# Performance work log

Measured on AMD Instinct MI355X. Metric: run time of the kernel, lower is better.

Reference implementation:

```python
import jax, jax.numpy as jnp
import numpy as np

B, T, D, H, L, FF, SPLIT = 2, 4096, 256, 4 * 0 + 8, 4, 1024, 2048
HD = D // H
EPS = 1e-5


def _layernorm(x, s, b):
    mu = jnp.mean(x, axis=-1, keepdims=True)
    var = jnp.mean(jnp.square(x - mu), axis=-1, keepdims=True)
    return (x - mu) * jax.lax.rsqrt(var + EPS) * s + b


def setup_inputs() -> dict:
    key = jax.random.key(0)
    ks = jax.random.split(key, 10)
    sc = 0.02
    inp = {
        "rows": jax.random.normal(ks[0], (B, T, D), jnp.float32),
        "train_target_embeddings": jax.random.normal(ks[1], (B, SPLIT, D), jnp.float32),
        "Wq": sc * jax.random.normal(ks[2], (L, D, D), jnp.float32),
        "bq": jnp.zeros((L, D), jnp.float32),
        "Wk": sc * jax.random.normal(ks[3], (L, D, D), jnp.float32),
        "bk": jnp.zeros((L, D), jnp.float32),
        "Wv": sc * jax.random.normal(ks[4], (L, D, D), jnp.float32),
        "bv": jnp.zeros((L, D), jnp.float32),
        "Wo": sc * jax.random.normal(ks[5], (L, D, D), jnp.float32),
        "bo": jnp.zeros((L, D), jnp.float32),
        "W1": sc * jax.random.normal(ks[6], (L, D, FF), jnp.float32),
        "b1": jnp.zeros((L, FF), jnp.float32),
        "W2": sc * jax.random.normal(ks[7], (L, FF, D), jnp.float32),
        "b2": jnp.zeros((L, D), jnp.float32),
        "ln1_s": jnp.ones((L, D), jnp.float32),
        "ln1_b": jnp.zeros((L, D), jnp.float32),
        "ln2_s": jnp.ones((L, D), jnp.float32),
        "ln2_b": jnp.zeros((L, D), jnp.float32),
        "split": SPLIT,
    }
    return inp


def reference(rows, train_target_embeddings, Wq, bq, Wk, bk, Wv, bv, Wo, bo,
              W1, b1, W2, b2, ln1_s, ln1_b, ln2_s, ln2_b, split):
    # residual add of train target embeddings onto the train rows
    x = rows.at[:, :split, :].add(train_target_embeddings)
    t = x.shape[1]
    # allowed mask: every query can see all train columns; test queries also see themselves
    key_is_train = jnp.arange(t) < split                      # [T]
    allowed = key_is_train[None, :] | jnp.eye(t, dtype=bool)  # [T,T]
    neg = jnp.asarray(-1e9, x.dtype)
    scale = 1.0 / np.sqrt(HD)
    n_layers = Wq.shape[0]
    for l in range(n_layers):
        # multi-head attention with structured mask
        q = (x @ Wq[l] + bq[l]).reshape(x.shape[0], t, H, HD)
        k = (x @ Wk[l] + bk[l]).reshape(x.shape[0], t, H, HD)
        v = (x @ Wv[l] + bv[l]).reshape(x.shape[0], t, H, HD)
        logits = jnp.einsum('bqhd,bkhd->bhqk', q, k) * scale
        logits = jnp.where(allowed[None, None], logits, neg)
        attn = jax.nn.softmax(logits, axis=-1)
        o = jnp.einsum('bhqk,bkhd->bqhd', attn, v).reshape(x.shape[0], t, D)
        x = _layernorm(x + (o @ Wo[l] + bo[l]), ln1_s[l], ln1_b[l])
        # feed-forward
        h = jax.nn.gelu(x @ W1[l] + b1[l])
        x = _layernorm(x + (h @ W2[l] + b2[l]), ln2_s[l], ln2_b[l])
    return x
```

## Files before the change

### kernel.cpp

```cpp
#include <hip/hip_runtime.h>
#include <cstdint>
#include <cstddef>

#define TSEQ 4096
#define BATCH 2
#define DIM 256
#define NHEAD 8
#define HDIM 32
#define NLAYER 4
#define FFDIM 1024
#define SPLITN 2048
#define MROWS (BATCH * TSEQ)

#define QSCALE 0.2550784545f

typedef __attribute__((ext_vector_type(4))) float f32x4;
typedef __attribute__((ext_vector_type(8))) short bf16x8;

__device__ __forceinline__ short f2bf(float f) {
  union { float f; uint32_t u; } v; v.f = f;
  uint32_t r = v.u + 0x7fffu + ((v.u >> 16) & 1u);
  return (short)(r >> 16);
}

__device__ __forceinline__ float bf2f(short s) {
  union { uint32_t u; float f; } v; v.u = ((uint32_t)(uint16_t)s) << 16;
  return v.f;
}

__device__ __forceinline__ float fast_exp2(float x) {
#if __has_builtin(__builtin_amdgcn_exp2f)
  return __builtin_amdgcn_exp2f(x);
#else
  float r;
  asm volatile("v_exp_f32 %0, %1\n\ts_nop 1" : "=v"(r) : "v"(x));
  return r;
#endif
}

__device__ __forceinline__ uint32_t pack2bf(float a, float b) {
  union { float f; uint32_t u; } ua, ub; ua.f = a; ub.f = b;
  return ((ua.u + 0x8000u) >> 16) | ((ub.u + 0x8000u) & 0xffff0000u);
}

__device__ __forceinline__ float gelu_f(float x) {
  float u = 0.7978845608f * x * (1.0f + 0.044715f * x * x);
  u = fminf(fmaxf(u, -20.f), 20.f);
  float e = fast_exp2(2.885390082f * u);
  float t = (e - 1.0f) / (e + 1.0f);
  return 0.5f * x * (1.0f + t);
}

#define AS1 __attribute__((address_space(1)))
#define AS3 __attribute__((address_space(3)))
__device__ __forceinline__ void gload16(const void* g, void* l) {
  __builtin_amdgcn_global_load_lds((AS1 void*)g, (AS3 void*)l, 16, 0, 0);
}

__global__ __launch_bounds__(256) void prep_w(
    const float* __restrict__ Wq, const float* __restrict__ Wk,
    const float* __restrict__ Wv, const float* __restrict__ Wo,
    const float* __restrict__ W1, const float* __restrict__ W2,
    short* __restrict__ qkvT, short* __restrict__ woT,
    short* __restrict__ w1T, short* __restrict__ w2T)
{
  const int NQKV = NLAYER * 768 * DIM;
  const int NO   = NLAYER * DIM * DIM;
  const int NF   = NLAYER * FFDIM * DIM;
  const int total = NQKV + NO + 2 * NF;
  for (int idx = blockIdx.x * 256 + threadIdx.x; idx < total; idx += gridDim.x * 256) {
    if (idx < NQKV) {
      const int l = idx / (768 * DIM);
      const int rem = idx - l * 768 * DIM;
      const int n = rem >> 8, k = rem & 255;
      const float* src = (n < 256) ? Wq : ((n < 512) ? Wk : Wv);
      qkvT[idx] = f2bf(src[((size_t)l * DIM + k) * DIM + (n & 255)]);
    } else if (idx < NQKV + NO) {
      const int j = idx - NQKV;
      const int l = j >> 16;
      const int rem = j & 65535;
      const int n = rem >> 8, k = rem & 255;
      woT[j] = f2bf(Wo[((size_t)l * DIM + k) * DIM + n]);
    } else if (idx < NQKV + NO + NF) {
      const int j = idx - NQKV - NO;
      const int l = j >> 18;
      const int rem = j & 262143;
      const int n = rem >> 8, k = rem & 255;
      w1T[j] = f2bf(W1[((size_t)l * DIM + k) * FFDIM + n]);
    } else {
      const int j = idx - NQKV - NO - NF;
      const int l = j >> 18;
      const int rem = j & 262143;
      const int n = rem >> 10, k = rem & 1023;
      w2T[j] = f2bf(W2[((size_t)l * FFDIM + k) * DIM + n]);
    }
  }
}

__global__ __launch_bounds__(256) void prep_x(
    const float* __restrict__ rows, const float* __restrict__ tte,
    float* __restrict__ xf, short* __restrict__ xb)
{
  const size_t idx = (size_t)blockIdx.x * 256 + threadIdx.x;
  float4 v = ((const float4*)rows)[idx];
  const size_t e = idx * 4;
  const int m = (int)(e >> 8);
  const int d = (int)(e & 255);
  const int t = m & (TSEQ - 1);
  const int bb = m >> 12;
  if (t < SPLITN) {
    const float4 a = ((const float4*)tte)[((size_t)bb * SPLITN + t) * (DIM / 4) + (d >> 2)];
    v.x += a.x; v.y += a.y; v.z += a.z; v.w += a.w;
  }
  ((float4*)xf)[idx] = v;
  short4 pk; pk.x = f2bf(v.x); pk.y = f2bf(v.y); pk.z = f2bf(v.z); pk.w = f2bf(v.w);
  ((short4*)xb)[idx] = pk;
}

#define GBM 128
#define GBN 64
#define GBK 64

template<int EPI>
__global__ __launch_bounds__(256, 4) void gemm_bt(
    const short* __restrict__ A, const short* __restrict__ BT,
    const float* __restrict__ bias0, const float* __restrict__ bias1,
    const float* __restrict__ bias2, void* __restrict__ Cout,
    int M, int N, int K)
{
  __shared__ short As[GBM * GBK];
  __shared__ short Bs[GBN * GBK];
  const int tid = threadIdx.x;
  const int lane = tid & 63;
  const int wave = tid >> 6;
  const int wm = wave & 1, wn = wave >> 1;
  const int col = lane & 15, quad = lane >> 4;

  const short* Ab = A + (size_t)blockIdx.x * GBM * K;
  const short* Bb = BT + (size_t)blockIdx.y * GBN * K;

  const f32x4 fz = {0.f, 0.f, 0.f, 0.f};
  f32x4 acc[4][2];
#pragma unroll
  for (int i = 0; i < 4; ++i)
#pragma unroll
    for (int j = 0; j < 2; ++j) acc[i][j] = fz;

  for (int k0 = 0; k0 < K; k0 += GBK) {
#pragma unroll
    for (int p = 0; p < 4; ++p) {
      const int i = p * 256 + tid;
      const int r = i >> 3, g = i & 7;
      gload16(Ab + (size_t)r * K + k0 + ((g ^ (r & 7)) * 8), &As[i * 8]);
    }
#pragma unroll
    for (int p = 0; p < 2; ++p) {
      const int i = p * 256 + tid;
      const int r = i >> 3, g = i & 7;
      gload16(Bb + (size_t)r * K + k0 + ((g ^ (r & 7)) * 8), &Bs[i * 8]);
    }
    __syncthreads();
#pragma unroll
    for (int ks = 0; ks < GBK; ks += 32) {
      bf16x8 af[4], bfr[2];
      const int gq = (ks >> 3) + quad;
#pragma unroll
      for (int tm = 0; tm < 4; ++tm) {
        const int row = wm * 64 + tm * 16 + col;
        af[tm] = *(const bf16x8*)&As[row * GBK + ((gq ^ (row & 7)) * 8)];
      }
#pragma unroll
      for (int tn = 0; tn < 2; ++tn) {
        const int row = wn * 32 + tn * 16 + col;
        bfr[tn] = *(const bf16x8*)&Bs[row * GBK + ((gq ^ (row & 7)) * 8)];
      }
#pragma unroll
      for (int tm = 0; tm < 4; ++tm)
#pragma unroll
        for (int tn = 0; tn < 2; ++tn)
          acc[tm][tn] = __builtin_amdgcn_mfma_f32_16x16x32_bf16(af[tm], bfr[tn], acc[tm][tn], 0, 0, 0);
    }
    __syncthreads();
  }

#pragma unroll
  for (int tm = 0; tm < 4; ++tm) {
    const int mbase = blockIdx.x * GBM + wm * 64 + tm * 16 + quad * 4;
#pragma unroll
    for (int tn = 0; tn < 2; ++tn) {
      const int n = blockIdx.y * GBN + wn * 32 + tn * 16 + col;
      float bv;
      if (EPI == 1) bv = (n < 256) ? bias0[n] : ((n < 512) ? bias1[n - 256] : bias2[n - 512]);
      else          bv = bias0[n];
#pragma unroll
      for (int r = 0; r < 4; ++r) {
        float v = acc[tm][tn][r] + bv;
        size_t off = (size_t)(mbase + r) * N + n;
        if (EPI == 1) {
          if (n < 256) v *= QSCALE;
          ((short*)Cout)[off] = f2bf(v);
        } else {
          ((short*)Cout)[off] = f2bf(gelu_f(v));
        }
      }
    }
  }
}

template<int MODE>
__global__ __launch_bounds__(256, 2) void gemm_ln(
    const short* __restrict__ A, const float* __restrict__ Opart,
    const float* __restrict__ lpart,
    const short* __restrict__ BT, const float* __restrict__ bias,
    const float* __restrict__ xres,
    const float* __restrict__ gs, const float* __restrict__ gb,
    float* __restrict__ xoutf, short* __restrict__ xoutb, int K)
{
  __shared__ short As[2][32 * 64];
  __shared__ short Bs[2][256 * 64];
  __shared__ float ssum[4][32], ssq[4][32];
  const int tid = threadIdx.x;
  const int lane = tid & 63;
  const int wave = tid >> 6;
  const int col = lane & 15, quad = lane >> 4;
  const int m0 = blockIdx.x * 32;

  const f32x4 fz = {0.f, 0.f, 0.f, 0.f};
  f32x4 acc[2][4];
#pragma unroll
  for (int i = 0; i < 2; ++i)
#pragma unroll
    for (int j = 0; j < 4; ++j) acc[i][j] = fz;

  const int arow = tid >> 3;
  const int agr  = tid & 7;
  const int grow = m0 + arow;
  const int asw  = (agr ^ (arow & 7)) * 8;

  float4 sa0, sa1, sc0, sc1; float sli = 0.f;

#define STAGE_B(k0_, buf_) do {                                              \
    _Pragma("unroll")                                                        \
    for (int p_ = 0; p_ < 8; ++p_) {                                         \
      const int i_ = p_ * 256 + tid;                                         \
      const int r_ = i_ >> 3, g_ = i_ & 7;                                   \
      gload16(BT + (size_t)r_ * K + (k0_) + ((g_ ^ (r_ & 7)) * 8),           \
              &Bs[buf_][i_ * 8]);                                            \
    } } while (0)

#define STAGE_A_ISSUE(k0_, buf_) do {                                        \
    if (MODE == 0) {                                                         \
      gload16(A + (size_t)grow * K + (k0_) + asw, &As[buf_][tid * 8]);       \
    } else {                                                                 \
      const int tt_ = grow & (TSEQ - 1), bb_ = grow >> 12;                   \
      const int head_ = ((k0_) >> 5) + (agr >= 4 ? 1 : 0);                   \
      const size_t lidx_ = (size_t)(bb_ * 8 + head_) * TSEQ + tt_;           \
      sli = lpart[lidx_] + lpart[(size_t)16 * TSEQ + lidx_];                 \
      const size_t ob_ = (size_t)grow * DIM + (k0_) + agr * 8;               \
      sa0 = *(const float4*)(Opart + ob_);                                   \
      sa1 = *(const float4*)(Opart + ob_ + 4);                               \
      sc0 = *(const float4*)(Opart + (size_t)MROWS * DIM + ob_);             \
      sc1 = *(const float4*)(Opart + (size_t)MROWS * DIM + ob_ + 4);         \
    } } while (0)

#define STAGE_A_WRITE(buf_) do {                                             \
    if (MODE == 1) {                                                         \
      const float li_ = 1.0f / sli;                                          \
      uint4 w_;                                                              \
      w_.x = pack2bf((sa0.x + sc0.x) * li_, (sa0.y + sc0.y) * li_);          \
      w_.y = pack2bf((sa0.z + sc0.z) * li_, (sa0.w + sc0.w) * li_);          \
      w_.z = pack2bf((sa1.x + sc1.x) * li_, (sa1.y + sc1.y) * li_);          \
      w_.w = pack2bf((sa1.z + sc1.z) * li_, (sa1.w + sc1.w) * li_);          \
      *(uint4*)&As[buf_][arow * 64 + asw] = w_;                              \
    } } while (0)

  const int NT = K / 64;
  STAGE_B(0, 0);
  STAGE_A_ISSUE(0, 0);
  STAGE_A_WRITE(0);
  __syncthreads();

  int cur = 0;
  for (int t = 0; t < NT; ++t) {
    if (t + 1 < NT) {
      STAGE_B((t + 1) * 64, cur ^ 1);
      STAGE_A_ISSUE((t + 1) * 64, cur ^ 1);
    }
#pragma unroll
    for (int ks = 0; ks < 64; ks += 32) {
      bf16x8 af[2], bfr[4];
      const int gq = (ks >> 3) + quad;
#pragma unroll
      for (int tm = 0; tm < 2; ++tm) {
        const int row = tm * 16 + col;
        af[tm] = *(const bf16x8*)&As[cur][row * 64 + ((gq ^ (row & 7)) * 8)];
      }
#pragma unroll
      for (int tn = 0; tn < 4; ++tn) {
        const int row = wave * 64 + tn * 16 + col;
        bfr[tn] = *(const bf16x8*)&Bs[cur][row * 64 + ((gq ^ (row & 7)) * 8)];
      }
#pragma unroll
      for (int tm = 0; tm < 2; ++tm)
#pragma unroll
        for (int tn = 0; tn < 4; ++tn)
          acc[tm][tn] = __builtin_amdgcn_mfma_f32_16x16x32_bf16(af[tm], bfr[tn], acc[tm][tn], 0, 0, 0);
    }
    if (t + 1 < NT) STAGE_A_WRITE(cur ^ 1);
    __syncthreads();
    cur ^= 1;
  }
#undef STAGE_B
#undef STAGE_A_ISSUE
#undef STAGE_A_WRITE

  const float* resb = xres + (size_t)m0 * DIM;
#pragma unroll
  for (int tn = 0; tn < 4; ++tn) {
    const int n = wave * 64 + tn * 16 + col;
    const float bv = bias[n];
#pragma unroll
    for (int tm = 0; tm < 2; ++tm)
#pragma unroll
      for (int r = 0; r < 4; ++r) {
        const int row = tm * 16 + quad * 4 + r;
        acc[tm][tn][r] += bv + resb[(size_t)row * DIM + n];
      }
  }

#pragma unroll
  for (int tm = 0; tm < 2; ++tm)
#pragma unroll
    for (int r = 0; r < 4; ++r) {
      float s = 0.f, q = 0.f;
#pragma unroll
      for (int tn = 0; tn < 4; ++tn) { const float v = acc[tm][tn][r]; s += v; q += v * v; }
      s += __shfl_xor(s, 1); q += __shfl_xor(q, 1);
      s += __shfl_xor(s, 2); q += __shfl_xor(q, 2);
      s += __shfl_xor(s, 4); q += __shfl_xor(q, 4);
      s += __shfl_xor(s, 8); q += __shfl_xor(q, 8);
      if (col == 0) { const int row = tm * 16 + quad * 4 + r; ssum[wave][row] = s; ssq[wave][row] = q; }
    }
  __syncthreads();
  if (tid < 32) {
    const float S = ssum[0][tid] + ssum[1][tid] + ssum[2][tid] + ssum[3][tid];
    const float Q = ssq[0][tid] + ssq[1][tid] + ssq[2][tid] + ssq[3][tid];
    const float mu = S * (1.0f / DIM);
    const float var = Q * (1.0f / DIM) - mu * mu;
    ssum[0][tid] = mu;
    ssq[0][tid] = rsqrtf(var + 1e-5f);
  }
  __syncthreads();

#pragma unroll
  for (int tm = 0; tm < 2; ++tm)
#pragma unroll
    for (int tn = 0; tn < 4; ++tn) {
      const int n = wave * 64 + tn * 16 + col;
      const float g = gs[n], bb = gb[n];
#pragma unroll
      for (int r = 0; r < 4; ++r) {
        const int row = tm * 16 + quad * 4 + r;
        const float out = (acc[tm][tn][r] - ssum[0][row]) * ssq[0][row] * g + bb;
        xoutf[(size_t)(m0 + row) * DIM + n] = out;
        xoutb[(size_t)(m0 + row) * DIM + n] = f2bf(out);
      }
    }
}

#define AKT 64
#define KSPL 1024
#define NKT (KSPL / AKT)

__global__ __launch_bounds__(256, 4) void attn_kernel(
    const short* __restrict__ qkv,
    float* __restrict__ Opart, float* __restrict__ lpart)
{
  __shared__ short Kbuf[2][AKT * HDIM];
  __shared__ short Vbuf[2][HDIM * AKT];
  __shared__ short Pall[4][32][72];
  __shared__ float Pdiag[4][16];

  const int tid = threadIdx.x;
  const int lane = tid & 63;
  const int wave = tid >> 6;
  const int col = lane & 15, quad = lane >> 4;
  const int bh = blockIdx.y;
  const int b = bh >> 3, h = bh & 7;
  const int hz = blockIdx.z;
  const int q0 = blockIdx.x * 128 + wave * 32;

  short (*P)[72] = Pall[wave];

  const short* qbase = qkv + (size_t)b * TSEQ * 768 + h * HDIM;
  const short* kbase = qbase + 256;
  const short* vcol  = qbase + 512;

  const short* ksrc = kbase + (size_t)(hz * KSPL + (tid & 63)) * 768 + (tid >> 6) * 8;
  const int vkey = tid & 63, vhg = tid >> 6;
  const int va = vkey >> 3, vb8 = vkey & 7;
  const short* vsrc = vcol + (size_t)(hz * KSPL + vkey) * 768 + vhg * 8;

  const bf16x8 qf0 = *(const bf16x8*)(qbase + (size_t)(q0 + col) * 768 + quad * 8);
  const bf16x8 qf1 = *(const bf16x8*)(qbase + (size_t)(q0 + 16 + col) * 768 + quad * 8);

  bf16x8 ones;
#pragma unroll
  for (int i = 0; i < 8; ++i) ones[i] = (short)0x3F80;

  const f32x4 fz = {0.f, 0.f, 0.f, 0.f};
  f32x4 o[2][2] = {{fz, fz}, {fz, fz}};
  f32x4 lacc[2] = {fz, fz};

  gload16(ksrc, &Kbuf[0][tid * 8]);
  {
    const bf16x8 v0 = *(const bf16x8*)vsrc;
#pragma unroll
    for (int j = 0; j < 8; ++j)
      Vbuf[0][(vhg * 8 + j) * 64 + ((va ^ j) * 8) + vb8] = v0[j];
  }
  bf16x8 vnext = *(const bf16x8*)(vsrc + (size_t)AKT * 768);

  int cur = 0;
  for (int t = 0; t < NKT; ++t) {
    __syncthreads();
    if (t + 1 < NKT) {
      gload16(ksrc + (size_t)(t + 1) * AKT * 768, &Kbuf[1 - cur][tid * 8]);
#pragma unroll
      for (int j = 0; j < 8; ++j)
        Vbuf[1 - cur][(vhg * 8 + j) * 64 + ((va ^ j) * 8) + vb8] = vnext[j];
      if (t + 2 < NKT) vnext = *(const bf16x8*)(vsrc + (size_t)(t + 2) * AKT * 768);
    }
    const short* kb = Kbuf[cur];
    const short* vb = Vbuf[cur];

#pragma unroll
    for (int st = 0; st < 4; ++st) {
      const bf16x8 kf = *(const bf16x8*)&kb[(quad * 64 + st * 16 + col) * 8];
      const f32x4 s0 = __builtin_amdgcn_mfma_f32_16x16x32_bf16(kf, qf0, fz, 0, 0, 0);
      const f32x4 s1 = __builtin_amdgcn_mfma_f32_16x16x32_bf16(kf, qf1, fz, 0, 0, 0);
      uint2 w0, w1;
      w0.x = pack2bf(fast_exp2(s0[0]), fast_exp2(s0[1]));
      w0.y = pack2bf(fast_exp2(s0[2]), fast_exp2(s0[3]));
      w1.x = pack2bf(fast_exp2(s1[0]), fast_exp2(s1[1]));
      w1.y = pack2bf(fast_exp2(s1[2]), fast_exp2(s1[3]));
      *(uint2*)&P[col][st * 16 + quad * 4] = w0;
      *(uint2*)&P[16 + col][st * 16 + quad * 4] = w1;
    }
    asm volatile("s_waitcnt lgkmcnt(0)" ::: "memory");

#pragma unroll
    for (int kh = 0; kh < 2; ++kh) {
      const bf16x8 pf0 = *(const bf16x8*)&P[col][kh * 32 + quad * 8];
      const bf16x8 pf1 = *(const bf16x8*)&P[16 + col][kh * 32 + quad * 8];
#pragma unroll
      for (int hh = 0; hh < 2; ++hh) {
        const int hd = hh * 16 + col;
        const bf16x8 vf = *(const bf16x8*)&vb[hd * AKT + (((kh * 4 + quad) ^ (hd & 7)) * 8)];
        o[0][hh] = __builtin_amdgcn_mfma_f32_16x16x32_bf16(pf0, vf, o[0][hh], 0, 0, 0);
        o[1][hh] = __builtin_amdgcn_mfma_f32_16x16x32_bf16(pf1, vf, o[1][hh], 0, 0, 0);
      }
      lacc[0] = __builtin_amdgcn_mfma_f32_16x16x32_bf16(pf0, ones, lacc[0], 0, 0, 0);
      lacc[1] = __builtin_amdgcn_mfma_f32_16x16x32_bf16(pf1, ones, lacc[1], 0, 0, 0);
    }
    cur ^= 1;
  }

  if (hz == 1 && blockIdx.x >= SPLITN / 128) {
#pragma unroll
    for (int qsub = 0; qsub < 2; ++qsub) {
      const int qd = q0 + qsub * 16;
      const bf16x8 qf = qsub ? qf1 : qf0;
      const bf16x8 kf = *(const bf16x8*)(kbase + (size_t)(qd + col) * 768 + quad * 8);
      const f32x4 sd = __builtin_amdgcn_mfma_f32_16x16x32_bf16(kf, qf, fz, 0, 0, 0);
      float ps = 0.f;
#pragma unroll
      for (int r = 0; r < 4; ++r)
        if (quad * 4 + r == col) ps = fast_exp2(sd[r]);
      if (quad == (col >> 2)) Pdiag[wave][col] = ps;
      asm volatile("s_waitcnt lgkmcnt(0)" ::: "memory");
      const f32x4 pv = *(const f32x4*)&Pdiag[wave][quad * 4];
#pragma unroll
      for (int r = 0; r < 4; ++r) {
        lacc[qsub][r] += pv[r];
        const size_t vrow = (size_t)(qd + quad * 4 + r) * 768;
#pragma unroll
        for (int hh = 0; hh < 2; ++hh)
          o[qsub][hh][r] += pv[r] * bf2f(vcol[vrow + hh * 16 + col]);
      }
      asm volatile("s_waitcnt lgkmcnt(0)" ::: "memory");
    }
  }

  float* Ob = Opart + (size_t)hz * MROWS * DIM;
  float* lb = lpart + (size_t)hz * 16 * TSEQ + (size_t)bh * TSEQ;
#pragma unroll
  for (int qsub = 0; qsub < 2; ++qsub) {
    const f32x4 la = lacc[qsub];
    const int qq = q0 + qsub * 16 + quad * 4;
    const int rowb = b * TSEQ + qq;
#pragma unroll
    for (int r = 0; r < 4; ++r) {
      if (col == 0) lb[qq + r] = la[r];
#pragma unroll
      for (int hh = 0; hh < 2; ++hh)
        Ob[(size_t)(rowb + r) * DIM + h * HDIM + hh * 16 + col] = o[qsub][hh][r];
    }
  }
}

extern "C" void kernel_launch(void* const* d_in, const int* in_sizes, int n_in,
                              void* d_out, int out_size, void* d_ws, size_t ws_size,
                              hipStream_t stream)
{
  const float* rows = (const float*)d_in[0];
  const float* tte  = (const float*)d_in[1];
  const float* Wq = (const float*)d_in[2];  const float* bq = (const float*)d_in[3];
  const float* Wk = (const float*)d_in[4];  const float* bk = (const float*)d_in[5];
  const float* Wv = (const float*)d_in[6];  const float* bv = (const float*)d_in[7];
  const float* Wo = (const float*)d_in[8];  const float* bo = (const float*)d_in[9];
  const float* W1 = (const float*)d_in[10]; const float* b1 = (const float*)d_in[11];
  const float* W2 = (const float*)d_in[12]; const float* b2 = (const float*)d_in[13];
  const float* ln1s = (const float*)d_in[14]; const float* ln1b = (const float*)d_in[15];
  const float* ln2s = (const float*)d_in[16]; const float* ln2b = (const float*)d_in[17];

  char* p = (char*)d_ws;
  float* xf   = (float*)p;  p += (size_t)MROWS * DIM * 4;
  short* xb   = (short*)p;  p += (size_t)MROWS * DIM * 2;
  short* qkv  = (short*)p;  p += (size_t)MROWS * 768 * 2;
  short* hb   = (short*)p;  p += (size_t)MROWS * FFDIM * 2;
  float* Opart = (float*)p; p += (size_t)2 * MROWS * DIM * 4;
  float* lpart = (float*)p; p += (size_t)2 * 16 * TSEQ * 4;
  short* qkvT = (short*)p;  p += (size_t)NLAYER * 768 * DIM * 2;
  short* woT  = (short*)p;  p += (size_t)NLAYER * DIM * DIM * 2;
  short* w1T  = (short*)p;  p += (size_t)NLAYER * FFDIM * DIM * 2;
  short* w2T  = (short*)p;  p += (size_t)NLAYER * DIM * FFDIM * 2;

  prep_w<<<2048, 256, 0, stream>>>(Wq, Wk, Wv, Wo, W1, W2, qkvT, woT, w1T, w2T);
  prep_x<<<MROWS * DIM / 4 / 256, 256, 0, stream>>>(rows, tte, xf, xb);

  for (int l = 0; l < NLAYER; ++l) {
    gemm_bt<1><<<dim3(MROWS / GBM, 768 / GBN), 256, 0, stream>>>(
        xb, qkvT + (size_t)l * 768 * DIM, bq + l * DIM, bk + l * DIM, bv + l * DIM,
        qkv, MROWS, 768, DIM);
    attn_kernel<<<dim3(TSEQ / 128, BATCH * NHEAD, 2), 256, 0, stream>>>(qkv, Opart, lpart);
    gemm_ln<1><<<MROWS / 32, 256, 0, stream>>>(
        nullptr, Opart, lpart, woT + (size_t)l * DIM * DIM, bo + l * DIM, xf,
        ln1s + l * DIM, ln1b + l * DIM, xf, xb, DIM);
    gemm_bt<3><<<dim3(MROWS / GBM, FFDIM / GBN), 256, 0, stream>>>(
        xb, w1T + (size_t)l * FFDIM * DIM, b1 + l * FFDIM, nullptr, nullptr,
        hb, MROWS, FFDIM, DIM);
    float* xo = (l == NLAYER - 1) ? (float*)d_out : xf;
    gemm_ln<0><<<MROWS / 32, 256, 0, stream>>>(
        hb, nullptr, nullptr, w2T + (size_t)l * DIM * FFDIM,
        b2 + l * DIM, xf, ln2s + l * DIM, ln2b + l * DIM, xo, xb, FFDIM);
  }
}
```

Measured before the change: 495.6 us.

## Widen GEMM tile with double-buffered LDS and load attention K into registers

The bias-epilogue GEMM moves from a 128x64 to a 128x128 tile and gets double-buffered shared memory, so the next K-slice is prefetched while the current one is multiplied. Occupancy drops from 4 to 2 blocks per SM and the grid gets smaller. The attention kernel no longer stages K through LDS: each wave loads its K fragments straight from global memory into registers and prefetches the next tile. This removes LDS traffic and LDS footprint, but raises register pressure, and each wave now issues its own redundant global loads of K.

After: 542.2 us. 9.4% more time.

```diff
diff --git a/kernel.cpp b/kernel.cpp
--- a/kernel.cpp
+++ b/kernel.cpp
@@ -118,18 +118,18 @@
 }
 
 #define GBM 128
-#define GBN 64
+#define GBN 128
 #define GBK 64
 
 template<int EPI>
-__global__ __launch_bounds__(256, 4) void gemm_bt(
+__global__ __launch_bounds__(256, 2) void gemm_bt(
     const short* __restrict__ A, const short* __restrict__ BT,
     const float* __restrict__ bias0, const float* __restrict__ bias1,
     const float* __restrict__ bias2, void* __restrict__ Cout,
     int M, int N, int K)
 {
-  __shared__ short As[GBM * GBK];
-  __shared__ short Bs[GBN * GBK];
+  __shared__ short As[2][GBM * GBK];
+  __shared__ short Bs[2][GBN * GBK];
   const int tid = threadIdx.x;
   const int lane = tid & 63;
   const int wave = tid >> 6;
@@ -140,55 +140,65 @@
   const short* Bb = BT + (size_t)blockIdx.y * GBN * K;
 
   const f32x4 fz = {0.f, 0.f, 0.f, 0.f};
-  f32x4 acc[4][2];
+  f32x4 acc[4][4];
 #pragma unroll
   for (int i = 0; i < 4; ++i)
 #pragma unroll
-    for (int j = 0; j < 2; ++j) acc[i][j] = fz;
-
+    for (int j = 0; j < 4; ++j) acc[i][j] = fz;
+
+#define STAGE_BT(k0_, buf_) do {                                             \
+    _Pragma("unroll")                                                        \
+    for (int p_ = 0; p_ < 4; ++p_) {                                         \
+      const int i_ = p_ * 256 + tid;                                         \
+      const int r_ = i_ >> 3, g_ = i_ & 7;                                   \
+      gload16(Ab + (size_t)r_ * K + (k0_) + ((g_ ^ (r_ & 7)) * 8),           \
+              &As[buf_][i_ * 8]);                                            \
+    }                                                                        \
+    _Pragma("unroll")                                                        \
+    for (int p_ = 0; p_ < 4; ++p_) {                                         \
+      const int i_ = p_ * 256 + tid;                                         \
+      const int r_ = i_ >> 3, g_ = i_ & 7;                                   \
+      gload16(Bb + (size_t)r_ * K + (k0_) + ((g_ ^ (r_ & 7)) * 8),           \
+              &Bs[buf_][i_ * 8]);                                            \
+    } } while (0)
+
+  STAGE_BT(0, 0);
+  __syncthreads();
+
+  int cur = 0;
   for (int k0 = 0; k0 < K; k0 += GBK) {
-#pragma unroll
-    for (int p = 0; p < 4; ++p) {
-      const int i = p * 256 + tid;
-      const int r = i >> 3, g = i & 7;
-      gload16(Ab + (size_t)r * K + k0 + ((g ^ (r & 7)) * 8), &As[i * 8]);
-    }
-#pragma unroll
-    for (int p = 0; p < 2; ++p) {
-      const int i = p * 256 + tid;
-      const int r = i >> 3, g = i & 7;
-      gload16(Bb + (size_t)r * K + k0 + ((g ^ (r & 7)) * 8), &Bs[i * 8]);
-    }
-    __syncthreads();
+    if (k0 + GBK < K) STAGE_BT(k0 + GBK, cur ^ 1);
 #pragma unroll
     for (int ks = 0; ks < GBK; ks += 32) {
-      bf16x8 af[4], bfr[2];
+      bf16x8 af[4], bfr[4];
       const int gq = (ks >> 3) + quad;
 #pragma unroll
       for (int tm = 0; tm < 4; ++tm) {
         const int row = wm * 64 + tm * 16 + col;
-        af[tm] = *(const bf16x8*)&As[row * GBK + ((gq ^ (row & 7)) * 8)];
-      }
-#pragma unroll
-      for (int tn = 0; tn < 2; ++tn) {
-        const int row = wn * 32 + tn * 16 + col;
-        bfr[tn] = *(const bf16x8*)&Bs[row * GBK + ((gq ^ (row & 7)) * 8)];
+        af[tm] = *(const bf16x8*)&As[cur][row * GBK + ((gq ^ (row & 7)) * 8)];
+      }
+#pragma unroll
+      for (int tn = 0; tn < 4; ++tn) {
+        const int row = wn * 64 + tn * 16 + col;
+        bfr[tn] = *(const bf16x8*)&Bs[cur][row * GBK + ((gq ^ (row & 7)) * 8)];
       }
 #pragma unroll
       for (int tm = 0; tm < 4; ++tm)
 #pragma unroll
-        for (int tn = 0; tn < 2; ++tn)
+        for (int tn = 0; tn < 4; ++tn)
           acc[tm][tn] = __builtin_amdgcn_mfma_f32_16x16x32_bf16(af[tm], bfr[tn], acc[tm][tn], 0, 0, 0);
     }
     __syncthreads();
-  }
+    cur ^= 1;
+  }
+#undef STAGE_BT
 
 #pragma unroll
   for (int tm = 0; tm < 4; ++tm) {
     const int mbase = blockIdx.x * GBM + wm * 64 + tm * 16 + quad * 4;
 #pragma unroll
-    for (int tn = 0; tn < 2; ++tn) {
-      const int n = blockIdx.y * GBN + wn * 32 + tn * 16 + col;
+    for (int tn = 0; tn < 4; ++tn) {
+      const int n = blockIdx.y * GBN + wn * 64 + tn * 16 + col;
       float bv;
       if (EPI == 1) bv = (n < 256) ? bias0[n] : ((n < 512) ? bias1[n - 256] : bias2[n - 512]);
       else          bv = bias0[n];
@@ -376,7 +386,6 @@
     const short* __restrict__ qkv,
     float* __restrict__ Opart, float* __restrict__ lpart)
 {
-  __shared__ short Kbuf[2][AKT * HDIM];
   __shared__ short Vbuf[2][HDIM * AKT];
   __shared__ short Pall[4][32][72];
   __shared__ float Pdiag[4][16];
@@ -396,7 +405,7 @@
   const short* kbase = qbase + 256;
   const short* vcol  = qbase + 512;
 
-  const short* ksrc = kbase + (size_t)(hz * KSPL + (tid & 63)) * 768 + (tid >> 6) * 8;
+  const short* kfs = kbase + (size_t)(hz * KSPL + col) * 768 + quad * 8;
   const int vkey = tid & 63, vhg = tid >> 6;
   const int va = vkey >> 3, vb8 = vkey & 7;
   const short* vsrc = vcol + (size_t)(hz * KSPL + vkey) * 768 + vhg * 8;
@@ -412,7 +421,10 @@
   f32x4 o[2][2] = {{fz, fz}, {fz, fz}};
   f32x4 lacc[2] = {fz, fz};
 
-  gload16(ksrc, &Kbuf[0][tid * 8]);
+  bf16x8 kf_cur[4], kf_nxt[4];
+#pragma unroll
+  for (int st = 0; st < 4; ++st)
+    kf_cur[st] = *(const bf16x8*)(kfs + (size_t)(st * 16) * 768);
   {
     const bf16x8 v0 = *(const bf16x8*)vsrc;
 #pragma unroll
@@ -425,18 +437,19 @@
   for (int t = 0; t < NKT; ++t) {
     __syncthreads();
     if (t + 1 < NKT) {
-      gload16(ksrc + (size_t)(t + 1) * AKT * 768, &Kbuf[1 - cur][tid * 8]);
 #pragma unroll
       for (int j = 0; j < 8; ++j)
         Vbuf[1 - cur][(vhg * 8 + j) * 64 + ((va ^ j) * 8) + vb8] = vnext[j];
       if (t + 2 < NKT) vnext = *(const bf16x8*)(vsrc + (size_t)(t + 2) * AKT * 768);
-    }
-    const short* kb = Kbuf[cur];
+#pragma unroll
+      for (int st = 0; st < 4; ++st)
+        kf_nxt[st] = *(const bf16x8*)(kfs + (size_t)((t + 1) * AKT + st * 16) * 768);
+    }
     const short* vb = Vbuf[cur];
 
 #pragma unroll
     for (int st = 0; st < 4; ++st) {
-      const bf16x8 kf = *(const bf16x8*)&kb[(quad * 64 + st * 16 + col) * 8];
+      const bf16x8 kf = kf_cur[st];
       const f32x4 s0 = __builtin_amdgcn_mfma_f32_16x16x32_bf16(kf, qf0, fz, 0, 0, 0);
       const f32x4 s1 = __builtin_amdgcn_mfma_f32_16x16x32_bf16(kf, qf1, fz, 0, 0, 0);
       uint2 w0, w1;
@@ -463,6 +476,8 @@
       lacc[0] = __builtin_amdgcn_mfma_f32_16x16x32_bf16(pf0, ones, lacc[0], 0, 0, 0);
       lacc[1] = __builtin_amdgcn_mfma_f32_16x16x32_bf16(pf1, ones, lacc[1], 0, 0, 0);
     }
+#pragma unroll
+    for (int st = 0; st < 4; ++st) kf_cur[st] = kf_nxt[st];
     cur ^= 1;
   }
 
```

## Keep attention probabilities in registers by permuting V layout to match MFMA output

Applied to the files above, without the earlier changes.

Removes the per-wave shared-memory P staging buffer and the lgkmcnt wait. The softmax probabilities from the QK MFMA are packed directly into registers as the A operand of the PV MFMA. To make the register layout line up, V's key order in LDS is permuted so each key matches the position the probability lands in. This saves LDS writes and reads and a sync point per tile, at the cost of more live registers and tighter coupling to the MFMA lane mapping.

After: 488.0 us. No clear change (-1.5%).

```diff
diff --git a/kernel.cpp b/kernel.cpp
--- a/kernel.cpp
+++ b/kernel.cpp
@@ -41,6 +41,11 @@
 __device__ __forceinline__ uint32_t pack2bf(float a, float b) {
   union { float f; uint32_t u; } ua, ub; ua.f = a; ub.f = b;
   return ((ua.u + 0x8000u) >> 16) | ((ub.u + 0x8000u) & 0xffff0000u);
+}
+
+__device__ __forceinline__ bf16x8 mk8(uint32_t a, uint32_t b, uint32_t c, uint32_t d) {
+  union { uint32_t u[4]; bf16x8 v; } x; x.u[0] = a; x.u[1] = b; x.u[2] = c; x.u[3] = d;
+  return x.v;
 }
 
 __device__ __forceinline__ float gelu_f(float x) {
@@ -378,7 +383,6 @@
 {
   __shared__ short Kbuf[2][AKT * HDIM];
   __shared__ short Vbuf[2][HDIM * AKT];
-  __shared__ short Pall[4][32][72];
   __shared__ float Pdiag[4][16];
 
   const int tid = threadIdx.x;
@@ -390,15 +394,15 @@
   const int hz = blockIdx.z;
   const int q0 = blockIdx.x * 128 + wave * 32;
 
-  short (*P)[72] = Pall[wave];
-
   const short* qbase = qkv + (size_t)b * TSEQ * 768 + h * HDIM;
   const short* kbase = qbase + 256;
   const short* vcol  = qbase + 512;
 
   const short* ksrc = kbase + (size_t)(hz * KSPL + (tid & 63)) * 768 + (tid >> 6) * 8;
   const int vkey = tid & 63, vhg = tid >> 6;
-  const int va = vkey >> 3, vb8 = vkey & 7;
+  const int vs = vkey >> 4, vqd = (vkey >> 2) & 3, vrr = vkey & 3;
+  const int vpos = (vs >> 1) * 32 + vqd * 8 + (vs & 1) * 4 + vrr;
+  const int vgs = vpos >> 3, vo8 = vpos & 7;
   const short* vsrc = vcol + (size_t)(hz * KSPL + vkey) * 768 + vhg * 8;
 
   const bf16x8 qf0 = *(const bf16x8*)(qbase + (size_t)(q0 + col) * 768 + quad * 8);
@@ -417,7 +421,7 @@
     const bf16x8 v0 = *(const bf16x8*)vsrc;
 #pragma unroll
     for (int j = 0; j < 8; ++j)
-      Vbuf[0][(vhg * 8 + j) * 64 + ((va ^ j) * 8) + vb8] = v0[j];
+      Vbuf[0][(vhg * 8 + j) * 64 + ((vgs ^ j) * 8) + vo8] = v0[j];
   }
   bf16x8 vnext = *(const bf16x8*)(vsrc + (size_t)AKT * 768);
 
@@ -428,31 +432,28 @@
       gload16(ksrc + (size_t)(t + 1) * AKT * 768, &Kbuf[1 - cur][tid * 8]);
 #pragma unroll
       for (int j = 0; j < 8; ++j)
-        Vbuf[1 - cur][(vhg * 8 + j) * 64 + ((va ^ j) * 8) + vb8] = vnext[j];
+        Vbuf[1 - cur][(vhg * 8 + j) * 64 + ((vgs ^ j) * 8) + vo8] = vnext[j];
       if (t + 2 < NKT) vnext = *(const bf16x8*)(vsrc + (size_t)(t + 2) * AKT * 768);
     }
     const short* kb = Kbuf[cur];
     const short* vb = Vbuf[cur];
 
+    uint32_t pw0[8], pw1[8];
 #pragma unroll
     for (int st = 0; st < 4; ++st) {
       const bf16x8 kf = *(const bf16x8*)&kb[(quad * 64 + st * 16 + col) * 8];
       const f32x4 s0 = __builtin_amdgcn_mfma_f32_16x16x32_bf16(kf, qf0, fz, 0, 0, 0);
       const f32x4 s1 = __builtin_amdgcn_mfma_f32_16x16x32_bf16(kf, qf1, fz, 0, 0, 0);
-      uint2 w0, w1;
-      w0.x = pack2bf(fast_exp2(s0[0]), fast_exp2(s0[1]));
-      w0.y = pack2bf(fast_exp2(s0[2]), fast_exp2(s0[3]));
-      w1.x = pack2bf(fast_exp2(s1[0]), fast_exp2(s1[1]));
-      w1.y = pack2bf(fast_exp2(s1[2]), fast_exp2(s1[3]));
-      *(uint2*)&P[col][st * 16 + quad * 4] = w0;
-      *(uint2*)&P[16 + col][st * 16 + quad * 4] = w1;
-    }
-    asm volatile("s_waitcnt lgkmcnt(0)" ::: "memory");
+      pw0[st * 2]     = pack2bf(fast_exp2(s0[0]), fast_exp2(s0[1]));
+      pw0[st * 2 + 1] = pack2bf(fast_exp2(s0[2]), fast_exp2(s0[3]));
+      pw1[st * 2]     = pack2bf(fast_exp2(s1[0]), fast_exp2(s1[1]));
+      pw1[st * 2 + 1] = pack2bf(fast_exp2(s1[2]), fast_exp2(s1[3]));
+    }
 
 #pragma unroll
     for (int kh = 0; kh < 2; ++kh) {
-      const bf16x8 pf0 = *(const bf16x8*)&P[col][kh * 32 + quad * 8];
-      const bf16x8 pf1 = *(const bf16x8*)&P[16 + col][kh * 32 + quad * 8];
+      const bf16x8 pf0 = mk8(pw0[kh * 4], pw0[kh * 4 + 1], pw0[kh * 4 + 2], pw0[kh * 4 + 3]);
+      const bf16x8 pf1 = mk8(pw1[kh * 4], pw1[kh * 4 + 1], pw1[kh * 4 + 2], pw1[kh * 4 + 3]);
 #pragma unroll
       for (int hh = 0; hh < 2; ++hh) {
         const int hd = hh * 16 + col;
```
